# Performance work log

Hardware: AMD Instinct MI355X
Metric: run time of the kernel (lower is better)

## Reference

```python
import jax, jax.numpy as jnp
import numpy as np

THETA_ALPHA = 160.0  # spatial bandwidth of bilateral kernel
THETA_BETA = 3.0     # color bandwidth of bilateral kernel
THETA_GAMMA = 3.0    # spatial bandwidth of spatial kernel
NUM_ITERS = 5        # mean-field iterations


def setup_inputs() -> dict:
    key = jax.random.key(0)
    ks = jax.random.split(key, 5)
    B, H, W, C = 1, 80, 80, 21
    unaries = jax.random.normal(ks[0], (B, H, W, C), dtype=jnp.float32)
    image = jax.random.uniform(ks[1], (B, H, W, 3), dtype=jnp.float32) * 255.0
    spatial_w = jax.random.normal(ks[2], (C, C), dtype=jnp.float32) * 0.1 + jnp.eye(C)
    bilateral_w = jax.random.normal(ks[3], (C, C), dtype=jnp.float32) * 0.1 + jnp.eye(C)
    compat = jax.random.normal(ks[4], (C, C), dtype=jnp.float32) * 0.1 - jnp.eye(C)
    return {"unaries": unaries, "image": image, "spatial_w": spatial_w,
            "bilateral_w": bilateral_w, "compat": compat}


def _gauss_kernel(feat):
    # feat: [N, F] -> dense Gaussian affinity exp(-0.5*||f_i - f_j||^2), [N, N]
    sq = jnp.sum(feat * feat, axis=-1)
    d2 = sq[:, None] + sq[None, :] - 2.0 * (feat @ feat.T)
    return jnp.exp(-0.5 * jnp.maximum(d2, 0.0))


def reference(unaries, image, spatial_w, bilateral_w, compat):
    B, H, W, C = unaries.shape
    N = H * W
    yy, xx = jnp.meshgrid(jnp.arange(H, dtype=jnp.float32),
                          jnp.arange(W, dtype=jnp.float32), indexing="ij")
    pos = jnp.stack([yy, xx], axis=-1).reshape(N, 2)          # [N, 2]
    rgb = image.reshape(N, 3)
    feat_s = pos / THETA_GAMMA                                 # spatial kernel features
    feat_b = jnp.concatenate([pos / THETA_ALPHA, rgb / THETA_BETA], axis=-1)
    Ks = _gauss_kernel(feat_s)                                 # [N, N]
    Kb = _gauss_kernel(feat_b)                                 # [N, N]
    norm_s = jnp.sum(Ks, axis=-1, keepdims=True)               # splat-of-ones normalization
    norm_b = jnp.sum(Kb, axis=-1, keepdims=True)
    u = unaries.reshape(N, C)
    q = u
    for _ in range(NUM_ITERS):
        p = jax.nn.softmax(q, axis=-1)                         # [N, C]
        msg = (Ks @ p) / norm_s @ spatial_w.T + (Kb @ p) / norm_b @ bilateral_w.T
        q = u - msg @ compat.T                                 # compatibility transform
    return q.reshape(B, H, W, C)
```

## Files before the change

kernel.cpp:

```cpp
#include <hip/hip_runtime.h>
#include <hip/hip_bf16.h>


#define HH 80
#define WW 80
#define NPIX 6400
#define CC 21
#define PP 24
#define NITER 5
#define NCAP 64
#define SADGATE 23u
#define RAD 14

__global__ void __launch_bounds__(1024) nbr_kernel(const float* __restrict__ image,
        const float* __restrict__ unaries,
        int* __restrict__ nbr_j, float* __restrict__ nbr_k, int* __restrict__ nbr_cnt,
        float* __restrict__ norm_b, float* __restrict__ Stab, float* __restrict__ p0) {
    __shared__ unsigned int cimg[NPIX];
    int tid = threadIdx.x;
    int bid = blockIdx.x;
    for (int px = tid; px < NPIX; px += 1024) {
        float r = image[px * 3 + 0], g = image[px * 3 + 1], b = image[px * 3 + 2];
        unsigned ur = (unsigned)(r + 0.5f), ug = (unsigned)(g + 0.5f), ub = (unsigned)(b + 0.5f);
        cimg[px] = ur | (ug << 8) | (ub << 16);
    }
    if (bid == 0 && tid < HH) {
        float s = 0.f;
        float t = (float)tid;
        for (int tp = 0; tp < HH; ++tp) {
            float d = t - (float)tp;
            s += __expf(-d * d * (1.0f / 18.0f));
        }
        Stab[tid] = s;
    }
    __syncthreads();
    int lane = tid & 63;
    int i = bid * 16 + (tid >> 6);
    unsigned ci = cimg[i];
    float eir = image[i * 3 + 0], eig = image[i * 3 + 1], eib = image[i * 3 + 2];
    float yi = (float)(i / WW), xi = (float)(i % WW);
    int base = 0;
    float ksum = 0.f;
    for (int j0 = 0; j0 < NPIX; j0 += 64) {
        int j = j0 + lane;
        unsigned cj = cimg[j];
#if __has_builtin(__builtin_amdgcn_sad_u8)
        unsigned sad = __builtin_amdgcn_sad_u8(ci, cj, 0u);
#else
        int dr = (int)(ci & 255u) - (int)(cj & 255u);
        int dg = (int)((ci >> 8) & 255u) - (int)((cj >> 8) & 255u);
        int db = (int)((ci >> 16) & 255u) - (int)((cj >> 16) & 255u);
        unsigned sad = (unsigned)(abs(dr) + abs(dg) + abs(db));
#endif
        bool pass = (sad <= SADGATE);
        unsigned long long mask = __ballot(pass);
        if (pass) {
            int slot = base + __popcll(mask & ((1ull << lane) - 1ull));
            if (slot < NCAP) {
                float er = eir - image[j * 3 + 0];
                float eg = eig - image[j * 3 + 1];
                float eb = eib - image[j * 3 + 2];
                float dy = (yi - (float)(j / WW)) * (1.0f / 160.0f);
                float dx = (xi - (float)(j % WW)) * (1.0f / 160.0f);
                float d2 = (er * er + eg * eg + eb * eb) * (1.0f / 9.0f) + dy * dy + dx * dx;
                float kk = __expf(-0.5f * d2);
                nbr_j[i * NCAP + slot] = j;
                nbr_k[i * NCAP + slot] = kk;
                ksum += kk;
            }
        }
        base += (int)__popcll(mask);
    }
    for (int off = 32; off > 0; off >>= 1) ksum += __shfl_down(ksum, off, 64);
    if (lane == 0) {
        nbr_cnt[i] = (base < NCAP) ? base : NCAP;
        norm_b[i] = ksum;
    }
    float v = (lane < CC) ? unaries[i * CC + lane] : -1e30f;
    float m = v;
    for (int off = 16; off > 0; off >>= 1) m = fmaxf(m, __shfl_down(m, off, 32));
    m = __shfl(m, 0, 32);
    float e = (lane < CC) ? __expf(v - m) : 0.f;
    float s = e;
    for (int off = 16; off > 0; off >>= 1) s += __shfl_down(s, off, 32);
    s = __shfl(s, 0, 32);
    if (lane < CC) p0[i * PP + lane] = e / s;
}

__global__ void __launch_bounds__(256) iter_kernel(const float* __restrict__ unaries,
        const float* __restrict__ pc,
        const int* __restrict__ nbr_j, const float* __restrict__ nbr_k,
        const int* __restrict__ nbr_cnt, const float* __restrict__ norm_b,
        const float* __restrict__ Stab,
        const float* __restrict__ sw, const float* __restrict__ bw,
        const float* __restrict__ ct,
        float* __restrict__ pn, float* __restrict__ out, int last) {
    __shared__ float lsw[CC * CC], lbw[CC * CC], lct[CC * CC];
    __shared__ float gl[RAD + 1];
    __shared__ float Sx[10];
    __shared__ float Syv;
    __shared__ float4 cy4[38 * 6];
    __shared__ float4 asb4[10 * 6], abb4[10 * 6];
    __shared__ float msgb[10 * CC], ebuf[10 * CC];
    __shared__ int   njl[10][NCAP];
    __shared__ float nkl[10][NCAP];
    __shared__ int   cnt_l[10];
    __shared__ float inorm_l[10];
    float* asb = (float*)asb4;
    float* abb = (float*)abb4;
    float* cyf = (float*)cy4;

    int tid = threadIdx.x;
    int y = blockIdx.x >> 3, seg = blockIdx.x & 7;
    int x0 = seg * 10;
    int xs = (x0 - RAD > 0) ? x0 - RAD : 0;
    int xe = (x0 + 10 + RAD < WW) ? x0 + 10 + RAD : WW;
    int extw = xe - xs;

    for (int idx = tid; idx < CC * CC; idx += 256) {
        lsw[idx] = sw[idx]; lbw[idx] = bw[idx]; lct[idx] = ct[idx];
    }
    if (tid < RAD + 1) { float d = (float)tid; gl[tid] = __expf(-d * d * (1.0f / 18.0f)); }
    if (tid >= 32 && tid < 42) {
        int xl = tid - 32;
        Sx[xl] = Stab[x0 + xl];
        int i = y * WW + x0 + xl;
        cnt_l[xl] = nbr_cnt[i];
        inorm_l[xl] = 1.0f / norm_b[i];
    }
    if (tid == 42) Syv = Stab[y];
    __syncthreads();

    int yp0 = (y - RAD > 0) ? y - RAD : 0;
    int yp1 = (y + RAD < HH - 1) ? y + RAD : HH - 1;
    const float4* pc4 = (const float4*)pc;
    for (int idx = tid; idx < extw * 6; idx += 256) {
        int xl = idx / 6, ch = idx % 6;
        int x = xs + xl;
        float4 s = {0.f, 0.f, 0.f, 0.f};
        for (int yp = yp0; yp <= yp1; ++yp) {
            int d = y - yp; if (d < 0) d = -d;
            float gv = gl[d];
            float4 v = pc4[(yp * WW + x) * 6 + ch];
            s.x += gv * v.x; s.y += gv * v.y; s.z += gv * v.z; s.w += gv * v.w;
        }
        cy4[idx] = s;
    }
    for (int idx = tid; idx < 10 * NCAP; idx += 256) {
        int px = idx / NCAP, sl = idx % NCAP;
        if (sl < cnt_l[px]) {
            int i = y * WW + x0 + px;
            njl[px][sl] = nbr_j[i * NCAP + sl];
            nkl[px][sl] = nbr_k[i * NCAP + sl];
        }
    }
    __syncthreads();

    for (int idx = tid; idx < 210 + 60; idx += 256) {
        if (idx < 210) {
            int xl = idx / CC, c = idx % CC;
            int x = x0 + xl;
            int q0 = (x - RAD > 0) ? x - RAD : 0;
            int q1 = (x + RAD < WW - 1) ? x + RAD : WW - 1;
            float s = 0.f;
            for (int xp = q0; xp <= q1; ++xp) {
                int d = x - xp; if (d < 0) d = -d;
                s += gl[d] * cyf[(xp - xs) * PP + c];
            }
            asb[xl * PP + c] = s / (Syv * Sx[xl]);
        } else {
            int g = idx - 210;
            int px = g / 6, ch = g % 6;
            int cnt = cnt_l[px];
            float4 acc = {0.f, 0.f, 0.f, 0.f};
            for (int n = 0; n < cnt; ++n) {
                int j = njl[px][n];
                float kk = nkl[px][n];
                float4 v = pc4[j * 6 + ch];
                acc.x += kk * v.x; acc.y += kk * v.y; acc.z += kk * v.z; acc.w += kk * v.w;
            }
            float inb = inorm_l[px];
            acc.x *= inb; acc.y *= inb; acc.z *= inb; acc.w *= inb;
            abb4[px * 6 + ch] = acc;
        }
    }
    __syncthreads();

    for (int idx = tid; idx < 210; idx += 256) {
        int xl = idx / CC, c = idx % CC;
        float m = 0.f;
        #pragma unroll
        for (int k = 0; k < CC; ++k)
            m += lsw[c * CC + k] * asb[xl * PP + k] + lbw[c * CC + k] * abb[xl * PP + k];
        msgb[idx] = m;
    }
    __syncthreads();

    for (int idx = tid; idx < 210; idx += 256) {
        int xl = idx / CC, c = idx % CC;
        int i = y * WW + x0 + xl;
        float m = 0.f;
        #pragma unroll
        for (int k = 0; k < CC; ++k) m += lct[c * CC + k] * msgb[xl * CC + k];
        float qv = unaries[i * CC + c] - m;
        if (last) out[i * CC + c] = qv;
        else ebuf[idx] = __expf(qv);
    }
    if (!last) {
        __syncthreads();
        for (int idx = tid; idx < 210; idx += 256) {
            int xl = idx / CC, c = idx % CC;
            int i = y * WW + x0 + xl;
            float s = 0.f;
            #pragma unroll
            for (int cc2 = 0; cc2 < CC; ++cc2) s += ebuf[xl * CC + cc2];
            pn[i * PP + c] = ebuf[idx] / s;
        }
    }
}

extern "C" void kernel_launch(void* const* d_in, const int* in_sizes, int n_in,
                              void* d_out, int out_size, void* d_ws, size_t ws_size,
                              hipStream_t stream) {
    const float* unaries = (const float*)d_in[0];
    const float* image   = (const float*)d_in[1];
    const float* sw      = (const float*)d_in[2];
    const float* bw      = (const float*)d_in[3];
    const float* ct      = (const float*)d_in[4];
    float* out = (float*)d_out;

    char* ws = (char*)d_ws;
    size_t off = 0;
    auto alloc = [&](size_t bytes) -> char* {
        char* p = ws + off;
        off += (bytes + 255) & ~(size_t)255;
        return p;
    };
    int*   nbr_j   = (int*)alloc((size_t)NPIX * NCAP * 4);
    float* nbr_k   = (float*)alloc((size_t)NPIX * NCAP * 4);
    int*   nbr_cnt = (int*)alloc((size_t)NPIX * 4);
    float* norm_b  = (float*)alloc((size_t)NPIX * 4);
    float* pA      = (float*)alloc((size_t)NPIX * PP * 4);
    float* pB      = (float*)alloc((size_t)NPIX * PP * 4);
    float* Stab    = (float*)alloc(HH * 4);
    (void)ws_size;

    nbr_kernel<<<400, 1024, 0, stream>>>(image, unaries, nbr_j, nbr_k, nbr_cnt,
                                         norm_b, Stab, pA);
    float* pc = pA;
    float* pn = pB;
    for (int t = 0; t < NITER; ++t) {
        iter_kernel<<<640, 256, 0, stream>>>(unaries, pc, nbr_j, nbr_k, nbr_cnt,
                                             norm_b, Stab, sw, bw, ct, pn, out,
                                             (t == NITER - 1) ? 1 : 0);
        float* tsw = pc; pc = pn; pn = tsw;
    }
}
```

Before: 161.5 us.

## Store probabilities in bf16, prefold compat into weights, process two rows per block

Stores the per-iteration probability buffers as bf16 and reads them as 8-wide short vectors, halving the gather traffic. Precomputes compat·spatial_w and compat·bilateral_w once in the neighbour kernel, so each iteration does one 21x21 matvec instead of two chained ones. Each iter block now handles two image rows, sharing the column-pass loads and launching 320 blocks instead of 640. It also pre-divides the bilateral weights by their norm, caps neighbours at 48 and splits the neighbour sum across two lanes. In exchange, bf16 rounding and the tighter neighbour cap can change accuracy.

Measured after the change: 160.5 us. No clear change (-0.6%).

```diff
diff --git a/kernel.cpp b/kernel.cpp
--- a/kernel.cpp
+++ b/kernel.cpp
@@ -1,5 +1,4 @@
 #include <hip/hip_runtime.h>
-#include <hip/hip_bf16.h>
 
 
 #define HH 80
@@ -9,13 +8,29 @@
 #define PP 24
 #define NITER 5
 #define NCAP 64
+#define SCAP 48
 #define SADGATE 23u
 #define RAD 14
 
+typedef short short8 __attribute__((ext_vector_type(8)));
+union H8 { short8 v; unsigned short u[8]; };
+
+__device__ __forceinline__ float bf2f(unsigned short h) {
+    return __uint_as_float(((unsigned)h) << 16);
+}
+__device__ __forceinline__ unsigned short f2bf(float f) {
+    unsigned u = __float_as_uint(f);
+    return (unsigned short)((u + 0x7fffu + ((u >> 16) & 1u)) >> 16);
+}
+
 __global__ void __launch_bounds__(1024) nbr_kernel(const float* __restrict__ image,
         const float* __restrict__ unaries,
+        const float* __restrict__ sw, const float* __restrict__ bw,
+        const float* __restrict__ ct,
         int* __restrict__ nbr_j, float* __restrict__ nbr_k, int* __restrict__ nbr_cnt,
-        float* __restrict__ norm_b, float* __restrict__ Stab, float* __restrict__ p0) {
+        float* __restrict__ norm_b, float* __restrict__ Stab,
+        float* __restrict__ csw_g, float* __restrict__ cbw_g,
+        unsigned short* __restrict__ p0) {
     __shared__ unsigned int cimg[NPIX];
     int tid = threadIdx.x;
     int bid = blockIdx.x;
@@ -24,14 +39,24 @@
         unsigned ur = (unsigned)(r + 0.5f), ug = (unsigned)(g + 0.5f), ub = (unsigned)(b + 0.5f);
         cimg[px] = ur | (ug << 8) | (ub << 16);
     }
-    if (bid == 0 && tid < HH) {
-        float s = 0.f;
-        float t = (float)tid;
-        for (int tp = 0; tp < HH; ++tp) {
-            float d = t - (float)tp;
-            s += __expf(-d * d * (1.0f / 18.0f));
-        }
-        Stab[tid] = s;
+    if (bid == 0) {
+        if (tid < HH) {
+            float s = 0.f;
+            float t = (float)tid;
+            for (int tp = 0; tp < HH; ++tp) {
+                float d = t - (float)tp;
+                s += __expf(-d * d * (1.0f / 18.0f));
+            }
+            Stab[tid] = s;
+        }
+        for (int idx = tid; idx < 2 * CC * CC; idx += 1024) {
+            int m = idx % (CC * CC);
+            int c = m / CC, k = m % CC;
+            const float* wmat = (idx < CC * CC) ? sw : bw;
+            float s = 0.f;
+            for (int mm = 0; mm < CC; ++mm) s += ct[c * CC + mm] * wmat[mm * CC + k];
+            if (idx < CC * CC) csw_g[m] = s; else cbw_g[m] = s;
+        }
     }
     __syncthreads();
     int lane = tid & 63;
@@ -84,137 +109,145 @@
     float s = e;
     for (int off = 16; off > 0; off >>= 1) s += __shfl_down(s, off, 32);
     s = __shfl(s, 0, 32);
-    if (lane < CC) p0[i * PP + lane] = e / s;
+    if (lane < PP) p0[i * PP + lane] = (lane < CC) ? f2bf(e / s) : (unsigned short)0;
 }
 
 __global__ void __launch_bounds__(256) iter_kernel(const float* __restrict__ unaries,
-        const float* __restrict__ pc,
+        const unsigned short* __restrict__ pc,
         const int* __restrict__ nbr_j, const float* __restrict__ nbr_k,
         const int* __restrict__ nbr_cnt, const float* __restrict__ norm_b,
         const float* __restrict__ Stab,
-        const float* __restrict__ sw, const float* __restrict__ bw,
-        const float* __restrict__ ct,
-        float* __restrict__ pn, float* __restrict__ out, int last) {
-    __shared__ float lsw[CC * CC], lbw[CC * CC], lct[CC * CC];
-    __shared__ float gl[RAD + 1];
-    __shared__ float Sx[10];
-    __shared__ float Syv;
-    __shared__ float4 cy4[38 * 6];
-    __shared__ float4 asb4[10 * 6], abb4[10 * 6];
-    __shared__ float msgb[10 * CC], ebuf[10 * CC];
-    __shared__ int   njl[10][NCAP];
-    __shared__ float nkl[10][NCAP];
-    __shared__ int   cnt_l[10];
-    __shared__ float inorm_l[10];
-    float* asb = (float*)asb4;
-    float* abb = (float*)abb4;
-    float* cyf = (float*)cy4;
+        const float* __restrict__ csw_g, const float* __restrict__ cbw_g,
+        unsigned short* __restrict__ pn, float* __restrict__ out, int last) {
+    __shared__ float lcsw[CC * CC], lcbw[CC * CC];
+    __shared__ float gl[16];
+    __shared__ float cy[2 * 38 * PP];
+    __shared__ float asb[20 * PP];
+    __shared__ float abb[2][20 * PP];
+    __shared__ float ebuf[20 * PP];
+    __shared__ int   njl[20][SCAP];
+    __shared__ float nkl[20][SCAP];
+    __shared__ int   cnt_l[20];
+    __shared__ float inv_ns[20];
 
     int tid = threadIdx.x;
-    int y = blockIdx.x >> 3, seg = blockIdx.x & 7;
-    int x0 = seg * 10;
+    int y0 = (blockIdx.x >> 3) * 2;
+    int x0 = (blockIdx.x & 7) * 10;
     int xs = (x0 - RAD > 0) ? x0 - RAD : 0;
     int xe = (x0 + 10 + RAD < WW) ? x0 + 10 + RAD : WW;
     int extw = xe - xs;
-
-    for (int idx = tid; idx < CC * CC; idx += 256) {
-        lsw[idx] = sw[idx]; lbw[idx] = bw[idx]; lct[idx] = ct[idx];
-    }
-    if (tid < RAD + 1) { float d = (float)tid; gl[tid] = __expf(-d * d * (1.0f / 18.0f)); }
-    if (tid >= 32 && tid < 42) {
-        int xl = tid - 32;
-        Sx[xl] = Stab[x0 + xl];
-        int i = y * WW + x0 + xl;
-        cnt_l[xl] = nbr_cnt[i];
-        inorm_l[xl] = 1.0f / norm_b[i];
-    }
-    if (tid == 42) Syv = Stab[y];
-    __syncthreads();
-
-    int yp0 = (y - RAD > 0) ? y - RAD : 0;
-    int yp1 = (y + RAD < HH - 1) ? y + RAD : HH - 1;
-    const float4* pc4 = (const float4*)pc;
-    for (int idx = tid; idx < extw * 6; idx += 256) {
-        int xl = idx / 6, ch = idx % 6;
-        int x = xs + xl;
-        float4 s = {0.f, 0.f, 0.f, 0.f};
-        for (int yp = yp0; yp <= yp1; ++yp) {
-            int d = y - yp; if (d < 0) d = -d;
-            float gv = gl[d];
-            float4 v = pc4[(yp * WW + x) * 6 + ch];
-            s.x += gv * v.x; s.y += gv * v.y; s.z += gv * v.z; s.w += gv * v.w;
-        }
-        cy4[idx] = s;
-    }
-    for (int idx = tid; idx < 10 * NCAP; idx += 256) {
-        int px = idx / NCAP, sl = idx % NCAP;
-        if (sl < cnt_l[px]) {
-            int i = y * WW + x0 + px;
+    const short8* pc8 = (const short8*)pc;
+
+    for (int idx = tid; idx < 2 * CC * CC; idx += 256) {
+        if (idx < CC * CC) lcsw[idx] = csw_g[idx];
+        else lcbw[idx - CC * CC] = cbw_g[idx - CC * CC];
+    }
+    if (tid < 16) { float d = (float)tid; gl[tid] = __expf(-d * d * (1.0f / 18.0f)); }
+    if (tid >= 32 && tid < 52) {
+        int px = tid - 32;
+        int yl = px / 10, xl = px % 10;
+        int i = (y0 + yl) * WW + x0 + xl;
+        int cnt = nbr_cnt[i]; if (cnt > SCAP) cnt = SCAP;
+        cnt_l[px] = cnt;
+        inv_ns[px] = 1.0f / (Stab[y0 + yl] * Stab[x0 + xl]);
+    }
+    for (int idx = tid; idx < 20 * SCAP; idx += 256) {
+        int px = idx / SCAP, sl = idx % SCAP;
+        int yl = px / 10, xl = px % 10;
+        int i = (y0 + yl) * WW + x0 + xl;
+        int cnt = nbr_cnt[i]; if (cnt > SCAP) cnt = SCAP;
+        if (sl < cnt) {
             njl[px][sl] = nbr_j[i * NCAP + sl];
-            nkl[px][sl] = nbr_k[i * NCAP + sl];
-        }
-    }
-    __syncthreads();
-
-    for (int idx = tid; idx < 210 + 60; idx += 256) {
-        if (idx < 210) {
-            int xl = idx / CC, c = idx % CC;
-            int x = x0 + xl;
-            int q0 = (x - RAD > 0) ? x - RAD : 0;
-            int q1 = (x + RAD < WW - 1) ? x + RAD : WW - 1;
-            float s = 0.f;
-            for (int xp = q0; xp <= q1; ++xp) {
-                int d = x - xp; if (d < 0) d = -d;
-                s += gl[d] * cyf[(xp - xs) * PP + c];
-            }
-            asb[xl * PP + c] = s / (Syv * Sx[xl]);
+            nkl[px][sl] = nbr_k[i * NCAP + sl] / norm_b[i];
+        }
+    }
+    __syncthreads();
+
+    int climit = extw * 3;
+    for (int idx = tid; idx < climit + 120; idx += 256) {
+        if (idx < climit) {
+            int xl = idx / 3, grp = idx % 3;
+            int x = xs + xl;
+            int ys_ = (y0 - RAD > 0) ? y0 - RAD : 0;
+            int ye_ = (y0 + 1 + RAD < HH - 1) ? y0 + 1 + RAD : HH - 1;
+            float a0[8] = {0,0,0,0,0,0,0,0}, a1[8] = {0,0,0,0,0,0,0,0};
+            for (int yp = ys_; yp <= ye_; ++yp) {
+                H8 h; h.v = pc8[(yp * WW + x) * 3 + grp];
+                int d0 = y0 - yp; if (d0 < 0) d0 = -d0;
+                int d1 = y0 + 1 - yp; if (d1 < 0) d1 = -d1;
+                float g0 = gl[d0], g1 = gl[d1];
+                #pragma unroll
+                for (int e = 0; e < 8; ++e) {
+                    float f = bf2f(h.u[e]);
+                    a0[e] += g0 * f; a1[e] += g1 * f;
+                }
+            }
+            #pragma unroll
+            for (int e = 0; e < 8; ++e) {
+                cy[(0 * 38 + xl) * PP + grp * 8 + e] = a0[e];
+                cy[(1 * 38 + xl) * PP + grp * 8 + e] = a1[e];
+            }
         } else {
-            int g = idx - 210;
-            int px = g / 6, ch = g % 6;
+            int g = idx - climit;
+            int px = g / 6, r = g % 6;
+            int grp = r >> 1, h = r & 1;
             int cnt = cnt_l[px];
-            float4 acc = {0.f, 0.f, 0.f, 0.f};
-            for (int n = 0; n < cnt; ++n) {
+            float acc[8] = {0,0,0,0,0,0,0,0};
+            for (int n = h; n < cnt; n += 2) {
                 int j = njl[px][n];
                 float kk = nkl[px][n];
-                float4 v = pc4[j * 6 + ch];
-                acc.x += kk * v.x; acc.y += kk * v.y; acc.z += kk * v.z; acc.w += kk * v.w;
-            }
-            float inb = inorm_l[px];
-            acc.x *= inb; acc.y *= inb; acc.z *= inb; acc.w *= inb;
-            abb4[px * 6 + ch] = acc;
-        }
-    }
-    __syncthreads();
-
-    for (int idx = tid; idx < 210; idx += 256) {
-        int xl = idx / CC, c = idx % CC;
+                H8 hv; hv.v = pc8[j * 3 + grp];
+                #pragma unroll
+                for (int e = 0; e < 8; ++e) acc[e] += kk * bf2f(hv.u[e]);
+            }
+            #pragma unroll
+            for (int e = 0; e < 8; ++e) abb[h][px * PP + grp * 8 + e] = acc[e];
+        }
+    }
+    __syncthreads();
+
+    for (int idx = tid; idx < 420; idx += 256) {
+        int px = idx / CC, c = idx % CC;
+        int yl = px / 10, xl = px % 10;
+        int x = x0 + xl;
+        int q0 = (x - RAD > 0) ? x - RAD : 0;
+        int q1 = (x + RAD < WW - 1) ? x + RAD : WW - 1;
+        float s = 0.f;
+        for (int xp = q0; xp <= q1; ++xp) {
+            int d = x - xp; if (d < 0) d = -d;
+            s += gl[d] * cy[(yl * 38 + (xp - xs)) * PP + c];
+        }
+        asb[px * PP + c] = s * inv_ns[px];
+    }
+    __syncthreads();
+
+    for (int idx = tid; idx < 420; idx += 256) {
+        int px = idx / CC, c = idx % CC;
+        int yl = px / 10, xl = px % 10;
+        int i = (y0 + yl) * WW + x0 + xl;
         float m = 0.f;
         #pragma unroll
         for (int k = 0; k < CC; ++k)
-            m += lsw[c * CC + k] * asb[xl * PP + k] + lbw[c * CC + k] * abb[xl * PP + k];
-        msgb[idx] = m;
-    }
-    __syncthreads();
-
-    for (int idx = tid; idx < 210; idx += 256) {
-        int xl = idx / CC, c = idx % CC;
-        int i = y * WW + x0 + xl;
-        float m = 0.f;
-        #pragma unroll
-        for (int k = 0; k < CC; ++k) m += lct[c * CC + k] * msgb[xl * CC + k];
+            m += lcsw[c * CC + k] * asb[px * PP + k]
+               + lcbw[c * CC + k] * (abb[0][px * PP + k] + abb[1][px * PP + k]);
         float qv = unaries[i * CC + c] - m;
         if (last) out[i * CC + c] = qv;
-        else ebuf[idx] = __expf(qv);
+        else ebuf[px * PP + c] = __expf(qv);
     }
     if (!last) {
         __syncthreads();
-        for (int idx = tid; idx < 210; idx += 256) {
-            int xl = idx / CC, c = idx % CC;
-            int i = y * WW + x0 + xl;
-            float s = 0.f;
-            #pragma unroll
-            for (int cc2 = 0; cc2 < CC; ++cc2) s += ebuf[xl * CC + cc2];
-            pn[i * PP + c] = ebuf[idx] / s;
+        for (int idx = tid; idx < 480; idx += 256) {
+            int px = idx / PP, c = idx % PP;
+            int yl = px / 10, xl = px % 10;
+            int i = (y0 + yl) * WW + x0 + xl;
+            if (c < CC) {
+                float s = 0.f;
+                #pragma unroll
+                for (int cc = 0; cc < CC; ++cc) s += ebuf[px * PP + cc];
+                pn[i * PP + c] = f2bf(ebuf[px * PP + c] / s);
+            } else {
+                pn[i * PP + c] = 0;
+            }
         }
     }
 }
@@ -240,19 +273,22 @@
     float* nbr_k   = (float*)alloc((size_t)NPIX * NCAP * 4);
     int*   nbr_cnt = (int*)alloc((size_t)NPIX * 4);
     float* norm_b  = (float*)alloc((size_t)NPIX * 4);
-    float* pA      = (float*)alloc((size_t)NPIX * PP * 4);
-    float* pB      = (float*)alloc((size_t)NPIX * PP * 4);
+    unsigned short* pA = (unsigned short*)alloc((size_t)NPIX * PP * 2);
+    unsigned short* pB = (unsigned short*)alloc((size_t)NPIX * PP * 2);
     float* Stab    = (float*)alloc(HH * 4);
+    float* csw_g   = (float*)alloc(CC * CC * 4);
+    float* cbw_g   = (float*)alloc(CC * CC * 4);
     (void)ws_size;
 
-    nbr_kernel<<<400, 1024, 0, stream>>>(image, unaries, nbr_j, nbr_k, nbr_cnt,
-                                         norm_b, Stab, pA);
-    float* pc = pA;
-    float* pn = pB;
+    nbr_kernel<<<400, 1024, 0, stream>>>(image, unaries, sw, bw, ct,
+                                         nbr_j, nbr_k, nbr_cnt, norm_b, Stab,
+                                         csw_g, cbw_g, pA);
+    unsigned short* pc = pA;
+    unsigned short* pn = pB;
     for (int t = 0; t < NITER; ++t) {
-        iter_kernel<<<640, 256, 0, stream>>>(unaries, pc, nbr_j, nbr_k, nbr_cnt,
-                                             norm_b, Stab, sw, bw, ct, pn, out,
+        iter_kernel<<<320, 256, 0, stream>>>(unaries, pc, nbr_j, nbr_k, nbr_cnt,
+                                             norm_b, Stab, csw_g, cbw_g, pn, out,
                                              (t == NITER - 1) ? 1 : 0);
-        float* tsw = pc; pc = pn; pn = tsw;
-    }
-}
+        unsigned short* tsw = pc; pc = pn; pn = tsw;
+    }
+}
```
